# Kernel tuning notes

Measured on AMD Instinct MI355X. Metric: run time of the kernel, lower is better.

## Reference

```python
import jax, jax.numpy as jnp
import numpy as np

B, S, IN, OUT, H, M = 16, 512, 512, 512, 8, 4
HF = OUT // H  # head_feats = 64


def setup_inputs() -> dict:
    key = jax.random.key(0)
    ks = jax.random.split(key, 12)
    std = 0.02
    queries = jax.random.normal(ks[0], (B, S, IN), jnp.float32)
    keys = jax.random.normal(ks[1], (B, S, IN), jnp.float32)
    timespans = jax.random.uniform(ks[2], (B, S), jnp.float32)
    # causal mask tiled over heads*batch, matching [H*B, S, S] score shape
    attention_masks = jnp.broadcast_to(jnp.tril(jnp.ones((S, S), jnp.float32)), (H * B, S, S))
    event_marks = jax.random.uniform(ks[3], (H * B, 1, S, M), jnp.float32)
    Wq = std * jax.random.normal(ks[4], (IN, OUT), jnp.float32)
    Wk = std * jax.random.normal(ks[5], (IN, OUT), jnp.float32)
    Wv = std * jax.random.normal(ks[6], (IN, OUT), jnp.float32)
    Wt = std * jax.random.normal(ks[7], (IN, OUT), jnp.float32)
    Wi = std * jax.random.normal(ks[8], (HF + 1, M * HF), jnp.float32)  # fc_i weight
    bi = jnp.zeros((M * HF,), jnp.float32)                               # fc_i bias
    weight_i = std * jax.random.normal(ks[9], (M, HF), jnp.float32)
    scale_i = jnp.zeros((M,), jnp.float32)
    return {"queries": queries, "keys": keys, "timespans": timespans,
            "attention_masks": attention_masks, "event_marks": event_marks,
            "Wq": Wq, "Wk": Wk, "Wv": Wv, "Wt": Wt, "Wi": Wi, "bi": bi,
            "weight_i": weight_i, "scale_i": scale_i}


def reference(queries, keys, timespans, attention_masks, event_marks,
              Wq, Wk, Wv, Wt, Wi, bi, weight_i, scale_i):
    # torch's cat(chunk(X, H, dim=2), dim=0) == [B,S,H,HF] -> [H,B,S,HF] -> flat h*B+b
    def split_heads(X):
        return X.reshape(B, S, H, HF).transpose(2, 0, 1, 3)  # [H,B,S,HF]

    Q = split_heads(queries @ Wq)
    K = split_heads(keys @ Wk)
    V = split_heads(keys @ Wv)
    T = split_heads(keys @ Wt)

    scores = jnp.einsum('hbqf,hbkf->hbqk', Q, K) / jnp.sqrt(jnp.float32(OUT))
    mask = attention_masks.reshape(H, B, S, S)
    scores = jnp.where(mask == 0.0, jnp.float32(-2 ** 32 + 1), scores)
    attn = jax.nn.softmax(scores, axis=-1)  # [H,B,Sq,Sk]

    E = jnp.einsum('hbqk,hbkf->hbqf', attn, T)  # events fed to intensity net

    # --- Hawkes intensities ---
    ts = jnp.broadcast_to(timespans[None, :, :, None], (H, B, S, 1))
    mu = jax.nn.sigmoid(jnp.concatenate([E, ts], axis=-1) @ Wi + bi)  # [H,B,S,M*HF]
    mu = mu.reshape(H, B, S, M, HF)  # chunk over marks along feature dim
    scale = jnp.exp(scale_i)  # [M]
    lam = jnp.einsum('hbsmf,mf->hbsm', mu, weight_i) / scale
    lam = scale * jnp.log1p(jnp.exp(lam))  # scaled softplus, [H,B,S,M]

    # mark_inty[h,b,q,k] = sum_m lam[h,b,q,m] * event_marks[h,b,k,m]
    em = event_marks.reshape(H, B, S, M)
    mark_inty = jnp.einsum('hbqm,hbkm->hbqk', lam, em)

    out = jnp.einsum('hbqk,hbkf->hbqf', attn * mark_inty, V)
    out = out.transpose(1, 2, 0, 3).reshape(B, S, OUT) + queries[..., :OUT]
    all_mark_inty = lam.reshape(H * B, S, M)
    return out, all_mark_inty
```

## Files before the change

kernel.cpp:

```cpp
#include <hip/hip_runtime.h>
#include <math.h>

typedef __attribute__((ext_vector_type(8))) short short8;
typedef __attribute__((ext_vector_type(4))) float f32x4;

static __device__ __forceinline__ unsigned short f2bf(float f) {
  unsigned int u = __float_as_uint(f);
  u += 0x7FFFu + ((u >> 16) & 1u);
  return (unsigned short)(u >> 16);
}

static __device__ __forceinline__ void cp16(void* lds, const void* g) {
  __builtin_amdgcn_global_load_lds((const __attribute__((address_space(1))) void*)g,
                                   (__attribute__((address_space(3))) void*)lds,
                                   16, 0, 0);
}

__global__ __launch_bounds__(256) void convert_k(
    const float* __restrict__ qin, const float* __restrict__ kin,
    const float* __restrict__ Wq, const float* __restrict__ Wk,
    const float* __restrict__ Wv, const float* __restrict__ Wt,
    const float* __restrict__ Wi,
    unsigned short* __restrict__ qbf, unsigned short* __restrict__ kbf,
    unsigned short* __restrict__ Wb, unsigned short* __restrict__ WiF)
{
  const int blk = blockIdx.x, tid = threadIdx.x;
  if (blk < 8192) {
    const float* src = (blk < 4096) ? qin : kin;
    unsigned short* dst = (blk < 4096) ? qbf : kbf;
    int i = ((blk & 4095) * 256 + tid) * 4;
    float4 v = *(const float4*)(src + i);
    ushort4 o;
    o.x = f2bf(v.x); o.y = f2bf(v.y); o.z = f2bf(v.z); o.w = f2bf(v.w);
    *(ushort4*)(dst + i) = o;
  } else if (blk < 12288) {
    int e = (blk - 8192) * 256 + tid;
    int which = e >> 18;
    int r = (e >> 9) & 511, c = e & 511;
    const float* W = (which == 0) ? Wq : (which == 1) ? Wk : (which == 2) ? Wv : Wt;
    Wb[which * 262144 + c * 512 + r] = f2bf(W[r * 512 + c]);
  } else {
    int e = (blk - 12288) * 256 + tid;
    int j = e & 7, ll = (e >> 3) & 63, r = e >> 9;
    int kk = r % 3, nt = r / 3;
    int col = nt * 16 + (ll & 15);
    int k = kk * 32 + (ll >> 4) * 8 + j;
    float val = (k < 64) ? Wi[k * 256 + col] : ((k == 64) ? Wi[16384 + col] : 0.0f);
    WiF[e] = f2bf(val);
  }
}

__global__ __launch_bounds__(256) void proj_mfma(
    const unsigned short* __restrict__ qin_bf, const unsigned short* __restrict__ kin_bf,
    const unsigned short* __restrict__ Wb,
    unsigned short* __restrict__ Qg, unsigned short* __restrict__ Kg,
    unsigned short* __restrict__ Vt, unsigned short* __restrict__ Tt)
{
  const int which = blockIdx.z;
  const unsigned short* A = (which == 0) ? qin_bf : kin_bf;
  const unsigned short* W = Wb + which * 262144;
  const int row0 = blockIdx.x * 128;
  const int col0 = blockIdx.y * 128;
  const int tid = threadIdx.x;
  const int wv = tid >> 6, l = tid & 63;
  const int quad = l >> 4, lc = l & 15;
  const int wm = wv >> 1, wn = wv & 1;

  __shared__ unsigned short Asm[128 * 32];
  __shared__ unsigned short Bsm[128 * 32];

  f32x4 acc[4][4] = {};
  const int c0 = tid, c1 = tid + 256;

  for (int k0 = 0; k0 < 512; k0 += 32) {
    __syncthreads();
    cp16(&Asm[c0 * 8], A + (size_t)(row0 + (c0 >> 2)) * 512 + k0 + (c0 & 3) * 8);
    cp16(&Asm[c1 * 8], A + (size_t)(row0 + (c1 >> 2)) * 512 + k0 + (c1 & 3) * 8);
    cp16(&Bsm[c0 * 8], W + (size_t)(col0 + (c0 >> 2)) * 512 + k0 + (c0 & 3) * 8);
    cp16(&Bsm[c1 * 8], W + (size_t)(col0 + (c1 >> 2)) * 512 + k0 + (c1 & 3) * 8);
    __syncthreads();
    short8 a[4], b[4];
#pragma unroll
    for (int mi = 0; mi < 4; ++mi)
      a[mi] = *(const short8*)&Asm[(wm * 64 + mi * 16 + lc) * 32 + quad * 8];
#pragma unroll
    for (int nj = 0; nj < 4; ++nj)
      b[nj] = *(const short8*)&Bsm[(wn * 64 + nj * 16 + lc) * 32 + quad * 8];
#pragma unroll
    for (int mi = 0; mi < 4; ++mi)
#pragma unroll
      for (int nj = 0; nj < 4; ++nj)
        acc[mi][nj] = __builtin_amdgcn_mfma_f32_16x16x32_bf16(a[mi], b[nj], acc[mi][nj], 0, 0, 0);
  }

  const int h = (col0 >> 6) + wn;
  const int bidx = row0 >> 9;
  const int hb = h * 16 + bidx;
  if (which < 2) {
    unsigned short* C = (which == 0) ? Qg : Kg;
#pragma unroll
    for (int mi = 0; mi < 4; ++mi) {
      int sbase = (row0 & 511) + wm * 64 + mi * 16 + quad * 4;
#pragma unroll
      for (int nj = 0; nj < 4; ++nj) {
        size_t base = (size_t)hb * 32768 + (size_t)sbase * 64 + nj * 16 + lc;
#pragma unroll
        for (int reg = 0; reg < 4; ++reg)
          C[base + (size_t)reg * 64] = f2bf(acc[mi][nj][reg]);
      }
    }
  } else {
    unsigned short* C = (which == 2) ? Vt : Tt;
#pragma unroll
    for (int mi = 0; mi < 4; ++mi) {
      int sbase = (row0 & 511) + wm * 64 + mi * 16 + quad * 4;
#pragma unroll
      for (int nj = 0; nj < 4; ++nj) {
        ushort4 o;
        o.x = f2bf(acc[mi][nj][0]); o.y = f2bf(acc[mi][nj][1]);
        o.z = f2bf(acc[mi][nj][2]); o.w = f2bf(acc[mi][nj][3]);
        *(ushort4*)&C[(size_t)hb * 32768 + (size_t)(nj * 16 + lc) * 512 + sbase] = o;
      }
    }
  }
}

__global__ __launch_bounds__(256) void attn_passA(
    const unsigned short* __restrict__ Qg, const unsigned short* __restrict__ Kg,
    const unsigned short* __restrict__ Ttg, const float* __restrict__ tsp,
    unsigned short* __restrict__ E96, float* __restrict__ mst, float* __restrict__ lst)
{
  const int qt = blockIdx.x, hb = blockIdx.y;
  const int q0 = qt << 6;
  const int tid = threadIdx.x, wv = tid >> 6, l = tid & 63;
  const int quad = l >> 4, lc = l & 15;

  __shared__ unsigned short Qs[64 * 64];
  __shared__ unsigned short Ks[64 * 64];
  __shared__ unsigned short Ts[64 * 64];
  __shared__ unsigned short Pl[4][16 * 72];

  const unsigned short* Qbase = Qg + (size_t)hb * 32768 + q0 * 64;
  cp16(&Qs[tid * 8], Qbase + tid * 8);
  cp16(&Qs[(tid + 256) * 8], Qbase + (tid + 256) * 8);

  f32x4 Eacc[4] = {};
  float mreg[4], lreg[4];
#pragma unroll
  for (int r = 0; r < 4; ++r) { mreg[r] = -3.0e38f; lreg[r] = 0.0f; }
  const float scl = 0.044194173824159216f;
  const int gqbase = q0 + wv * 16 + quad * 4;

  for (int kt = 0; kt <= qt; ++kt) {
    const int k0 = kt << 6;
    __syncthreads();
    const unsigned short* Kbase = Kg + (size_t)hb * 32768 + k0 * 64;
    cp16(&Ks[tid * 8], Kbase + tid * 8);
    cp16(&Ks[(tid + 256) * 8], Kbase + (tid + 256) * 8);
    const unsigned short* Tbase = Ttg + (size_t)hb * 32768 + k0;
    cp16(&Ts[tid * 8], Tbase + (size_t)(tid >> 3) * 512 + (tid & 7) * 8);
    cp16(&Ts[(tid + 256) * 8], Tbase + (size_t)((tid + 256) >> 3) * 512 + ((tid + 256) & 7) * 8);
    __syncthreads();

    f32x4 sc[4] = {};
#pragma unroll
    for (int kk = 0; kk < 2; ++kk) {
      short8 a = *(const short8*)&Qs[(wv * 16 + lc) * 64 + kk * 32 + quad * 8];
#pragma unroll
      for (int nj = 0; nj < 4; ++nj) {
        short8 b = *(const short8*)&Ks[(nj * 16 + lc) * 64 + kk * 32 + quad * 8];
        sc[nj] = __builtin_amdgcn_mfma_f32_16x16x32_bf16(a, b, sc[nj], 0, 0, 0);
      }
    }
    const bool diag = (kt == qt);
    float sm[4][4], alpha[4];
#pragma unroll
    for (int nj = 0; nj < 4; ++nj)
#pragma unroll
      for (int reg = 0; reg < 4; ++reg) {
        float v = sc[nj][reg] * scl;
        if (diag && (k0 + nj * 16 + lc) > (gqbase + reg)) v = -3.0e38f;
        sm[nj][reg] = v;
      }
#pragma unroll
    for (int reg = 0; reg < 4; ++reg) {
      float tmax = fmaxf(fmaxf(sm[0][reg], sm[1][reg]), fmaxf(sm[2][reg], sm[3][reg]));
#pragma unroll
      for (int off = 1; off < 16; off <<= 1) tmax = fmaxf(tmax, __shfl_xor(tmax, off));
      float mold = mreg[reg];
      float mn = fmaxf(mold, tmax);
      float al = __expf(mold - mn);
      float ts = 0.0f;
#pragma unroll
      for (int nj = 0; nj < 4; ++nj) {
        float p = __expf(sm[nj][reg] - mn);
        sm[nj][reg] = p;
        ts += p;
      }
#pragma unroll
      for (int off = 1; off < 16; off <<= 1) ts += __shfl_xor(ts, off);
      lreg[reg] = lreg[reg] * al + ts;
      mreg[reg] = mn;
      alpha[reg] = al;
    }
#pragma unroll
    for (int fj = 0; fj < 4; ++fj)
#pragma unroll
      for (int reg = 0; reg < 4; ++reg) Eacc[fj][reg] *= alpha[reg];
#pragma unroll
    for (int nj = 0; nj < 4; ++nj)
#pragma unroll
      for (int reg = 0; reg < 4; ++reg)
        Pl[wv][(quad * 4 + reg) * 72 + nj * 16 + lc] = f2bf(sm[nj][reg]);
#pragma unroll
    for (int kk = 0; kk < 2; ++kk) {
      short8 a = *(const short8*)&Pl[wv][lc * 72 + kk * 32 + quad * 8];
#pragma unroll
      for (int fj = 0; fj < 4; ++fj) {
        short8 b = *(const short8*)&Ts[(fj * 16 + lc) * 64 + kk * 32 + quad * 8];
        Eacc[fj] = __builtin_amdgcn_mfma_f32_16x16x32_bf16(a, b, Eacc[fj], 0, 0, 0);
      }
    }
  }

  unsigned short* Eb = E96 + ((size_t)hb * 512 + gqbase) * 96;
#pragma unroll
  for (int reg = 0; reg < 4; ++reg) {
    float inv = 1.0f / lreg[reg];
    unsigned short* rp = Eb + (size_t)reg * 96;
#pragma unroll
    for (int fj = 0; fj < 4; ++fj)
      rp[fj * 16 + lc] = f2bf(Eacc[fj][reg] * inv);
    float tsv = (lc == 0) ? tsp[(hb & 15) * 512 + gqbase + reg] : 0.0f;
    rp[64 + lc] = f2bf(tsv);
    rp[80 + lc] = 0;
  }
  if (lc == 0) {
#pragma unroll
    for (int reg = 0; reg < 4; ++reg) {
      mst[(size_t)hb * 512 + gqbase + reg] = mreg[reg];
      lst[(size_t)hb * 512 + gqbase + reg] = lreg[reg];
    }
  }
}

__global__ __launch_bounds__(256) void intensity_mfma(
    const unsigned short* __restrict__ E96, const unsigned short* __restrict__ WiF,
    const float* __restrict__ bi, const float* __restrict__ wim,
    const float* __restrict__ sci,
    float* __restrict__ lamws, float* __restrict__ lamout)
{
  const int tid = threadIdx.x, wv = tid >> 6, l = tid & 63;
  const int quad = l >> 4, lc = l & 15;
  __shared__ unsigned short WiS[24576];
#pragma unroll
  for (int i = 0; i < 12; ++i)
    cp16(&WiS[(tid + i * 256) * 8], WiF + (tid + i * 256) * 8);

  float bv[16], wmv[16];
#pragma unroll
  for (int nt = 0; nt < 16; ++nt) {
    bv[nt] = bi[nt * 16 + lc];
    wmv[nt] = wim[nt * 16 + lc];
  }
  const float scv = __expf(sci[lc & 3]);
  __syncthreads();

  for (int s = 0; s < 2; ++s) {
    const int row0 = ((blockIdx.x * 4 + wv) * 2 + s) * 16;
    f32x4 acc[16] = {};
#pragma unroll
    for (int kk = 0; kk < 3; ++kk) {
      short8 a = *(const short8*)(E96 + (size_t)(row0 + lc) * 96 + kk * 32 + quad * 8);
#pragma unroll
      for (int nt = 0; nt < 16; ++nt) {
        short8 b = *(const short8*)&WiS[((nt * 3 + kk) * 64 + l) * 8];
        acc[nt] = __builtin_amdgcn_mfma_f32_16x16x32_bf16(a, b, acc[nt], 0, 0, 0);
      }
    }
    float lam4[4][4] = {};
#pragma unroll
    for (int nt = 0; nt < 16; ++nt) {
#pragma unroll
      for (int reg = 0; reg < 4; ++reg) {
        float z = acc[nt][reg] + bv[nt];
        float mu = 1.0f / (1.0f + __expf(-z));
        lam4[reg][nt >> 2] += mu * wmv[nt];
      }
    }
#pragma unroll
    for (int reg = 0; reg < 4; ++reg)
#pragma unroll
      for (int m = 0; m < 4; ++m)
#pragma unroll
        for (int off = 1; off < 16; off <<= 1)
          lam4[reg][m] += __shfl_xor(lam4[reg][m], off);
    if (lc < 4) {
#pragma unroll
      for (int reg = 0; reg < 4; ++reg) {
        float z = lam4[reg][lc] / scv;
        float sp = (z > 20.0f) ? z : log1pf(__expf(z));
        float lv = scv * sp;
        size_t idx = (size_t)(row0 + quad * 4 + reg) * 4 + lc;
        lamws[idx] = lv;
        lamout[idx] = lv;
      }
    }
  }
}

__global__ __launch_bounds__(256) void attn_passB(
    const unsigned short* __restrict__ Qg, const unsigned short* __restrict__ Kg,
    const unsigned short* __restrict__ Vtg,
    const float* __restrict__ mst, const float* __restrict__ lst,
    const float* __restrict__ lam, const float* __restrict__ em,
    const float* __restrict__ queries, float* __restrict__ out)
{
  const int qt = blockIdx.x, hb = blockIdx.y;
  const int q0 = qt << 6;
  const int tid = threadIdx.x, wv = tid >> 6, l = tid & 63;
  const int quad = l >> 4, lc = l & 15;

  __shared__ unsigned short Qs[64 * 64];
  __shared__ unsigned short Ks[64 * 64];
  __shared__ unsigned short Vs[64 * 64];
  __shared__ unsigned short Pl[4][16 * 72];
  __shared__ float emS[64 * 4];

  const unsigned short* Qbase = Qg + (size_t)hb * 32768 + q0 * 64;
  cp16(&Qs[tid * 8], Qbase + tid * 8);
  cp16(&Qs[(tid + 256) * 8], Qbase + (tid + 256) * 8);

  const int gqbase = q0 + wv * 16 + quad * 4;
  float mr[4], li[4];
  float4 lamv[4];
#pragma unroll
  for (int reg = 0; reg < 4; ++reg) {
    size_t r = (size_t)hb * 512 + gqbase + reg;
    mr[reg] = mst[r];
    li[reg] = 1.0f / lst[r];
    lamv[reg] = *(const float4*)&lam[r * 4];
  }
  f32x4 Oacc[4] = {};
  const float scl = 0.044194173824159216f;

  for (int kt = 0; kt <= qt; ++kt) {
    const int k0 = kt << 6;
    __syncthreads();
    const unsigned short* Kbase = Kg + (size_t)hb * 32768 + k0 * 64;
    cp16(&Ks[tid * 8], Kbase + tid * 8);
    cp16(&Ks[(tid + 256) * 8], Kbase + (tid + 256) * 8);
    const unsigned short* Vbase = Vtg + (size_t)hb * 32768 + k0;
    cp16(&Vs[tid * 8], Vbase + (size_t)(tid >> 3) * 512 + (tid & 7) * 8);
    cp16(&Vs[(tid + 256) * 8], Vbase + (size_t)((tid + 256) >> 3) * 512 + ((tid + 256) & 7) * 8);
    emS[tid] = em[(size_t)hb * 2048 + k0 * 4 + tid];
    __syncthreads();

    f32x4 sc[4] = {};
#pragma unroll
    for (int kk = 0; kk < 2; ++kk) {
      short8 a = *(const short8*)&Qs[(wv * 16 + lc) * 64 + kk * 32 + quad * 8];
#pragma unroll
      for (int nj = 0; nj < 4; ++nj) {
        short8 b = *(const short8*)&Ks[(nj * 16 + lc) * 64 + kk * 32 + quad * 8];
        sc[nj] = __builtin_amdgcn_mfma_f32_16x16x32_bf16(a, b, sc[nj], 0, 0, 0);
      }
    }
    const bool diag = (kt == qt);
#pragma unroll
    for (int nj = 0; nj < 4; ++nj) {
      int col = nj * 16 + lc;
      float4 emv = *(const float4*)&emS[col * 4];
#pragma unroll
      for (int reg = 0; reg < 4; ++reg) {
        float v = sc[nj][reg] * scl;
        float p = (diag && (k0 + col) > (gqbase + reg))
                      ? 0.0f : __expf(v - mr[reg]) * li[reg];
        float mk = lamv[reg].x * emv.x + lamv[reg].y * emv.y +
                   lamv[reg].z * emv.z + lamv[reg].w * emv.w;
        Pl[wv][(quad * 4 + reg) * 72 + col] = f2bf(p * mk);
      }
    }
#pragma unroll
    for (int kk = 0; kk < 2; ++kk) {
      short8 a = *(const short8*)&Pl[wv][lc * 72 + kk * 32 + quad * 8];
#pragma unroll
      for (int fj = 0; fj < 4; ++fj) {
        short8 b = *(const short8*)&Vs[(fj * 16 + lc) * 64 + kk * 32 + quad * 8];
        Oacc[fj] = __builtin_amdgcn_mfma_f32_16x16x32_bf16(a, b, Oacc[fj], 0, 0, 0);
      }
    }
  }

  const int h = hb >> 4, bidx = hb & 15;
#pragma unroll
  for (int reg = 0; reg < 4; ++reg) {
    size_t o = (size_t)bidx * 262144 + (size_t)(gqbase + reg) * 512 + h * 64 + lc;
#pragma unroll
    for (int fj = 0; fj < 4; ++fj)
      out[o + fj * 16] = Oacc[fj][reg] + queries[o + fj * 16];
  }
}

extern "C" void kernel_launch(void* const* d_in, const int* in_sizes, int n_in,
                              void* d_out, int out_size, void* d_ws, size_t ws_size,
                              hipStream_t stream)
{
  (void)in_sizes; (void)n_in; (void)out_size; (void)ws_size;
  const float* queries = (const float*)d_in[0];
  const float* keys    = (const float*)d_in[1];
  const float* tsp     = (const float*)d_in[2];
  const float* em      = (const float*)d_in[4];
  const float* Wq      = (const float*)d_in[5];
  const float* Wk      = (const float*)d_in[6];
  const float* Wv      = (const float*)d_in[7];
  const float* Wt      = (const float*)d_in[8];
  const float* Wi      = (const float*)d_in[9];
  const float* bi      = (const float*)d_in[10];
  const float* wim     = (const float*)d_in[11];
  const float* sci     = (const float*)d_in[12];
  float* out = (float*)d_out;

  char* w = (char*)d_ws;
  unsigned short* Qg     = (unsigned short*)(w + 0);
  unsigned short* Kg     = (unsigned short*)(w + 8388608);
  unsigned short* Vt     = (unsigned short*)(w + 16777216);
  unsigned short* Tt     = (unsigned short*)(w + 25165824);
  unsigned short* E96    = (unsigned short*)(w + 33554432);
  float*          mst    = (float*)(w + 46137344);
  float*          lst    = (float*)(w + 46399488);
  float*          lam    = (float*)(w + 46661632);
  unsigned short* qin_bf = (unsigned short*)(w + 47710208);
  unsigned short* kin_bf = (unsigned short*)(w + 56098816);
  unsigned short* Wb     = (unsigned short*)(w + 64487424);
  unsigned short* WiF    = (unsigned short*)(w + 66584576);

  convert_k<<<12384, 256, 0, stream>>>(queries, keys, Wq, Wk, Wv, Wt, Wi,
                                       qin_bf, kin_bf, Wb, WiF);
  proj_mfma<<<dim3(64, 4, 4), 256, 0, stream>>>(qin_bf, kin_bf, Wb, Qg, Kg, Vt, Tt);
  attn_passA<<<dim3(8, 128), 256, 0, stream>>>(Qg, Kg, Tt, tsp, E96, mst, lst);
  intensity_mfma<<<512, 256, 0, stream>>>(E96, WiF, bi, wim, sci,
                                          lam, out + 4194304);
  attn_passB<<<dim3(8, 128), 256, 0, stream>>>(Qg, Kg, Vt, mst, lst, lam, em,
                                               queries, out);
}
```

Measured before the change: 340.6 us.

## Fuse attention pass A, intensity net, and pass B into one balanced causal kernel

Merges the two attention passes and the intensity MLP into one kernel, so the E96, m/l statistics and lambda intermediates never go through global memory and two launches disappear. Each block handles a pair of query tiles (qt and 7-qt) to even out causal work across blocks. It also drops online-softmax max tracking and exponentiates raw scaled scores, relying on scores staying small enough not to overflow. The weight transpose in the conversion kernel now goes through a shared-memory tiled transpose, replacing the strided scalar writes.

```diff
diff --git a/kernel.cpp b/kernel.cpp
--- a/kernel.cpp
+++ b/kernel.cpp
@@ -24,6 +24,7 @@
     unsigned short* __restrict__ qbf, unsigned short* __restrict__ kbf,
     unsigned short* __restrict__ Wb, unsigned short* __restrict__ WiF)
 {
+  __shared__ unsigned short tr[64 * 68];
   const int blk = blockIdx.x, tid = threadIdx.x;
   if (blk < 8192) {
     const float* src = (blk < 4096) ? qin : kin;
@@ -33,14 +34,31 @@
     ushort4 o;
     o.x = f2bf(v.x); o.y = f2bf(v.y); o.z = f2bf(v.z); o.w = f2bf(v.w);
     *(ushort4*)(dst + i) = o;
-  } else if (blk < 12288) {
-    int e = (blk - 8192) * 256 + tid;
-    int which = e >> 18;
-    int r = (e >> 9) & 511, c = e & 511;
+  } else if (blk < 8448) {
+    int t = blk - 8192;
+    int which = t >> 6, tile = t & 63;
+    int r0 = (tile >> 3) << 6, c0 = (tile & 7) << 6;
     const float* W = (which == 0) ? Wq : (which == 1) ? Wk : (which == 2) ? Wv : Wt;
-    Wb[which * 262144 + c * 512 + r] = f2bf(W[r * 512 + c]);
+    const int rr = tid >> 4, cc = (tid & 15) << 2;
+#pragma unroll
+    for (int u = 0; u < 4; ++u) {
+      int r = rr + u * 16;
+      float4 v = *(const float4*)(W + (size_t)(r0 + r) * 512 + c0 + cc);
+      tr[(cc + 0) * 68 + r] = f2bf(v.x);
+      tr[(cc + 1) * 68 + r] = f2bf(v.y);
+      tr[(cc + 2) * 68 + r] = f2bf(v.z);
+      tr[(cc + 3) * 68 + r] = f2bf(v.w);
+    }
+    __syncthreads();
+    unsigned short* dst = Wb + which * 262144;
+#pragma unroll
+    for (int u = 0; u < 4; ++u) {
+      int c = rr + u * 16;
+      ushort4 o = *(const ushort4*)&tr[c * 68 + cc];
+      *(ushort4*)(dst + (size_t)(c0 + c) * 512 + r0 + cc) = o;
+    }
   } else {
-    int e = (blk - 12288) * 256 + tid;
+    int e = (blk - 8448) * 256 + tid;
     int j = e & 7, ll = (e >> 3) & 63, r = e >> 9;
     int kk = r % 3, nt = r / 3;
     int col = nt * 16 + (ll & 15);
@@ -125,280 +143,203 @@
   }
 }
 
-__global__ __launch_bounds__(256) void attn_passA(
+__global__ __launch_bounds__(256) void attn_fused(
     const unsigned short* __restrict__ Qg, const unsigned short* __restrict__ Kg,
-    const unsigned short* __restrict__ Ttg, const float* __restrict__ tsp,
-    unsigned short* __restrict__ E96, float* __restrict__ mst, float* __restrict__ lst)
+    const unsigned short* __restrict__ Vtg, const unsigned short* __restrict__ Ttg,
+    const unsigned short* __restrict__ WiF,
+    const float* __restrict__ bi, const float* __restrict__ wim,
+    const float* __restrict__ sci, const float* __restrict__ tsp,
+    const float* __restrict__ em, const float* __restrict__ queries,
+    float* __restrict__ out, float* __restrict__ lamout)
 {
-  const int qt = blockIdx.x, hb = blockIdx.y;
-  const int q0 = qt << 6;
+  const int hb = blockIdx.y;
   const int tid = threadIdx.x, wv = tid >> 6, l = tid & 63;
   const int quad = l >> 4, lc = l & 15;
 
-  __shared__ unsigned short Qs[64 * 64];
-  __shared__ unsigned short Ks[64 * 64];
-  __shared__ unsigned short Ts[64 * 64];
-  __shared__ unsigned short Pl[4][16 * 72];
-
-  const unsigned short* Qbase = Qg + (size_t)hb * 32768 + q0 * 64;
-  cp16(&Qs[tid * 8], Qbase + tid * 8);
-  cp16(&Qs[(tid + 256) * 8], Qbase + (tid + 256) * 8);
-
-  f32x4 Eacc[4] = {};
-  float mreg[4], lreg[4];
-#pragma unroll
-  for (int r = 0; r < 4; ++r) { mreg[r] = -3.0e38f; lreg[r] = 0.0f; }
+  __shared__ unsigned short Qs[4096];
+  __shared__ unsigned short Ks[4096];
+  __shared__ unsigned short TVs[4096];
+  __shared__ unsigned short Wl[4][16 * 104];
+  __shared__ float emS[256];
+
   const float scl = 0.044194173824159216f;
-  const int gqbase = q0 + wv * 16 + quad * 4;
-
-  for (int kt = 0; kt <= qt; ++kt) {
-    const int k0 = kt << 6;
+  float scm[4];
+#pragma unroll
+  for (int m = 0; m < 4; ++m) scm[m] = __expf(sci[m]);
+
+  for (int half = 0; half < 2; ++half) {
+    const int qt = half ? (7 - blockIdx.x) : blockIdx.x;
+    const int q0 = qt << 6;
+    const int gqbase = q0 + wv * 16 + quad * 4;
     __syncthreads();
-    const unsigned short* Kbase = Kg + (size_t)hb * 32768 + k0 * 64;
-    cp16(&Ks[tid * 8], Kbase + tid * 8);
-    cp16(&Ks[(tid + 256) * 8], Kbase + (tid + 256) * 8);
-    const unsigned short* Tbase = Ttg + (size_t)hb * 32768 + k0;
-    cp16(&Ts[tid * 8], Tbase + (size_t)(tid >> 3) * 512 + (tid & 7) * 8);
-    cp16(&Ts[(tid + 256) * 8], Tbase + (size_t)((tid + 256) >> 3) * 512 + ((tid + 256) & 7) * 8);
-    __syncthreads();
-
-    f32x4 sc[4] = {};
-#pragma unroll
-    for (int kk = 0; kk < 2; ++kk) {
-      short8 a = *(const short8*)&Qs[(wv * 16 + lc) * 64 + kk * 32 + quad * 8];
+    const unsigned short* Qbase = Qg + (size_t)hb * 32768 + q0 * 64;
+    cp16(&Qs[tid * 8], Qbase + tid * 8);
+    cp16(&Qs[(tid + 256) * 8], Qbase + (tid + 256) * 8);
+
+    f32x4 Eacc[4] = {};
+    float lsum[4] = {0.f, 0.f, 0.f, 0.f};
+
+    for (int kt = 0; kt <= qt; ++kt) {
+      const int k0 = kt << 6;
+      __syncthreads();
+      const unsigned short* Kbase = Kg + (size_t)hb * 32768 + k0 * 64;
+      cp16(&Ks[tid * 8], Kbase + tid * 8);
+      cp16(&Ks[(tid + 256) * 8], Kbase + (tid + 256) * 8);
+      const unsigned short* Tbase = Ttg + (size_t)hb * 32768 + k0;
+      cp16(&TVs[tid * 8], Tbase + (size_t)(tid >> 3) * 512 + (tid & 7) * 8);
+      cp16(&TVs[(tid + 256) * 8], Tbase + (size_t)((tid + 256) >> 3) * 512 + ((tid + 256) & 7) * 8);
+      __syncthreads();
+
+      f32x4 sc[4] = {};
+#pragma unroll
+      for (int kk = 0; kk < 2; ++kk) {
+        short8 a = *(const short8*)&Qs[(wv * 16 + lc) * 64 + kk * 32 + quad * 8];
+#pragma unroll
+        for (int nj = 0; nj < 4; ++nj) {
+          short8 b = *(const short8*)&Ks[(nj * 16 + lc) * 64 + kk * 32 + quad * 8];
+          sc[nj] = __builtin_amdgcn_mfma_f32_16x16x32_bf16(a, b, sc[nj], 0, 0, 0);
+        }
+      }
+      const bool diag = (kt == qt);
 #pragma unroll
       for (int nj = 0; nj < 4; ++nj) {
-        short8 b = *(const short8*)&Ks[(nj * 16 + lc) * 64 + kk * 32 + quad * 8];
-        sc[nj] = __builtin_amdgcn_mfma_f32_16x16x32_bf16(a, b, sc[nj], 0, 0, 0);
-      }
-    }
-    const bool diag = (kt == qt);
-    float sm[4][4], alpha[4];
-#pragma unroll
-    for (int nj = 0; nj < 4; ++nj)
+        int col = nj * 16 + lc;
+#pragma unroll
+        for (int reg = 0; reg < 4; ++reg) {
+          float pv = __expf(sc[nj][reg] * scl);
+          if (diag && (k0 + col) > (gqbase + reg)) pv = 0.0f;
+          lsum[reg] += pv;
+          Wl[wv][(quad * 4 + reg) * 104 + col] = f2bf(pv);
+        }
+      }
+#pragma unroll
+      for (int kk = 0; kk < 2; ++kk) {
+        short8 a = *(const short8*)&Wl[wv][lc * 104 + kk * 32 + quad * 8];
+#pragma unroll
+        for (int fj = 0; fj < 4; ++fj) {
+          short8 b = *(const short8*)&TVs[(fj * 16 + lc) * 64 + kk * 32 + quad * 8];
+          Eacc[fj] = __builtin_amdgcn_mfma_f32_16x16x32_bf16(a, b, Eacc[fj], 0, 0, 0);
+        }
+      }
+    }
+
+    float inv[4];
+#pragma unroll
+    for (int reg = 0; reg < 4; ++reg) {
+      float s = lsum[reg];
+#pragma unroll
+      for (int off = 1; off < 16; off <<= 1) s += __shfl_xor(s, off);
+      inv[reg] = 1.0f / s;
+    }
+
+#pragma unroll
+    for (int reg = 0; reg < 4; ++reg) {
+      unsigned short* rp = &Wl[wv][(quad * 4 + reg) * 104];
+#pragma unroll
+      for (int fj = 0; fj < 4; ++fj)
+        rp[fj * 16 + lc] = f2bf(Eacc[fj][reg] * inv[reg]);
+      float tsv = (lc == 0) ? tsp[(hb & 15) * 512 + gqbase + reg] : 0.0f;
+      rp[64 + lc] = f2bf(tsv);
+      rp[80 + lc] = 0;
+    }
+
+    f32x4 iacc[16] = {};
+#pragma unroll
+    for (int kk = 0; kk < 3; ++kk) {
+      short8 a = *(const short8*)&Wl[wv][lc * 104 + kk * 32 + quad * 8];
+#pragma unroll
+      for (int nt = 0; nt < 16; ++nt) {
+        short8 b = *(const short8*)(WiF + ((nt * 3 + kk) * 64 + l) * 8);
+        iacc[nt] = __builtin_amdgcn_mfma_f32_16x16x32_bf16(a, b, iacc[nt], 0, 0, 0);
+      }
+    }
+    float lam4[4][4] = {};
+#pragma unroll
+    for (int nt = 0; nt < 16; ++nt) {
+      float bvv = bi[nt * 16 + lc];
+      float wmv = wim[nt * 16 + lc];
 #pragma unroll
       for (int reg = 0; reg < 4; ++reg) {
-        float v = sc[nj][reg] * scl;
-        if (diag && (k0 + nj * 16 + lc) > (gqbase + reg)) v = -3.0e38f;
-        sm[nj][reg] = v;
-      }
+        float mu = 1.0f / (1.0f + __expf(-(iacc[nt][reg] + bvv)));
+        lam4[reg][nt >> 2] += mu * wmv;
+      }
+    }
+#pragma unroll
+    for (int reg = 0; reg < 4; ++reg)
+#pragma unroll
+      for (int m = 0; m < 4; ++m) {
+        float s = lam4[reg][m];
+#pragma unroll
+        for (int off = 1; off < 16; off <<= 1) s += __shfl_xor(s, off);
+        float z = s / scm[m];
+        float sp = (z > 20.0f) ? z : log1pf(__expf(z));
+        lam4[reg][m] = scm[m] * sp;
+      }
+    if (lc < 4) {
+#pragma unroll
+      for (int reg = 0; reg < 4; ++reg) {
+        float v = (lc == 0) ? lam4[reg][0] : (lc == 1) ? lam4[reg][1]
+                : (lc == 2) ? lam4[reg][2] : lam4[reg][3];
+        lamout[((size_t)hb * 512 + gqbase + reg) * 4 + lc] = v;
+      }
+    }
+
+    f32x4 Oacc[4] = {};
+    for (int kt = 0; kt <= qt; ++kt) {
+      const int k0 = kt << 6;
+      __syncthreads();
+      const unsigned short* Kbase = Kg + (size_t)hb * 32768 + k0 * 64;
+      cp16(&Ks[tid * 8], Kbase + tid * 8);
+      cp16(&Ks[(tid + 256) * 8], Kbase + (tid + 256) * 8);
+      const unsigned short* Vbase = Vtg + (size_t)hb * 32768 + k0;
+      cp16(&TVs[tid * 8], Vbase + (size_t)(tid >> 3) * 512 + (tid & 7) * 8);
+      cp16(&TVs[(tid + 256) * 8], Vbase + (size_t)((tid + 256) >> 3) * 512 + ((tid + 256) & 7) * 8);
+      emS[tid] = em[(size_t)hb * 2048 + k0 * 4 + tid];
+      __syncthreads();
+
+      f32x4 sc[4] = {};
+#pragma unroll
+      for (int kk = 0; kk < 2; ++kk) {
+        short8 a = *(const short8*)&Qs[(wv * 16 + lc) * 64 + kk * 32 + quad * 8];
+#pragma unroll
+        for (int nj = 0; nj < 4; ++nj) {
+          short8 b = *(const short8*)&Ks[(nj * 16 + lc) * 64 + kk * 32 + quad * 8];
+          sc[nj] = __builtin_amdgcn_mfma_f32_16x16x32_bf16(a, b, sc[nj], 0, 0, 0);
+        }
+      }
+      const bool diag = (kt == qt);
+#pragma unroll
+      for (int nj = 0; nj < 4; ++nj) {
+        int col = nj * 16 + lc;
+        float4 emv = *(const float4*)&emS[col * 4];
+#pragma unroll
+        for (int reg = 0; reg < 4; ++reg) {
+          float pv = (diag && (k0 + col) > (gqbase + reg))
+                         ? 0.0f : __expf(sc[nj][reg] * scl) * inv[reg];
+          float mk = lam4[reg][0] * emv.x + lam4[reg][1] * emv.y +
+                     lam4[reg][2] * emv.z + lam4[reg][3] * emv.w;
+          Wl[wv][(quad * 4 + reg) * 104 + col] = f2bf(pv * mk);
+        }
+      }
+#pragma unroll
+      for (int kk = 0; kk < 2; ++kk) {
+        short8 a = *(const short8*)&Wl[wv][lc * 104 + kk * 32 + quad * 8];
+#pragma unroll
+        for (int fj = 0; fj < 4; ++fj) {
+          short8 b = *(const short8*)&TVs[(fj * 16 + lc) * 64 + kk * 32 + quad * 8];
+          Oacc[fj] = __builtin_amdgcn_mfma_f32_16x16x32_bf16(a, b, Oacc[fj], 0, 0, 0);
+        }
+      }
+    }
+
+    const int h = hb >> 4, bidx = hb & 15;
 #pragma unroll
     for (int reg = 0; reg < 4; ++reg) {
-      float tmax = fmaxf(fmaxf(sm[0][reg], sm[1][reg]), fmaxf(sm[2][reg], sm[3][reg]));
-#pragma unroll
-      for (int off = 1; off < 16; off <<= 1) tmax = fmaxf(tmax, __shfl_xor(tmax, off));
-      float mold = mreg[reg];
-      float mn = fmaxf(mold, tmax);
-      float al = __expf(mold - mn);
-      float ts = 0.0f;
-#pragma unroll
-      for (int nj = 0; nj < 4; ++nj) {
-        float p = __expf(sm[nj][reg] - mn);
-        sm[nj][reg] = p;
-        ts += p;
-      }
-#pragma unroll
-      for (int off = 1; off < 16; off <<= 1) ts += __shfl_xor(ts, off);
-      lreg[reg] = lreg[reg] * al + ts;
-      mreg[reg] = mn;
-      alpha[reg] = al;
-    }
-#pragma unroll
-    for (int fj = 0; fj < 4; ++fj)
-#pragma unroll
-      for (int reg = 0; reg < 4; ++reg) Eacc[fj][reg] *= alpha[reg];
-#pragma unroll
-    for (int nj = 0; nj < 4; ++nj)
-#pragma unroll
-      for (int reg = 0; reg < 4; ++reg)
-        Pl[wv][(quad * 4 + reg) * 72 + nj * 16 + lc] = f2bf(sm[nj][reg]);
-#pragma unroll
-    for (int kk = 0; kk < 2; ++kk) {
-      short8 a = *(const short8*)&Pl[wv][lc * 72 + kk * 32 + quad * 8];
-#pragma unroll
-      for (int fj = 0; fj < 4; ++fj) {
-        short8 b = *(const short8*)&Ts[(fj * 16 + lc) * 64 + kk * 32 + quad * 8];
-        Eacc[fj] = __builtin_amdgcn_mfma_f32_16x16x32_bf16(a, b, Eacc[fj], 0, 0, 0);
-      }
-    }
-  }
-
-  unsigned short* Eb = E96 + ((size_t)hb * 512 + gqbase) * 96;
-#pragma unroll
-  for (int reg = 0; reg < 4; ++reg) {
-    float inv = 1.0f / lreg[reg];
-    unsigned short* rp = Eb + (size_t)reg * 96;
-#pragma unroll
-    for (int fj = 0; fj < 4; ++fj)
-      rp[fj * 16 + lc] = f2bf(Eacc[fj][reg] * inv);
-    float tsv = (lc == 0) ? tsp[(hb & 15) * 512 + gqbase + reg] : 0.0f;
-    rp[64 + lc] = f2bf(tsv);
-    rp[80 + lc] = 0;
-  }
-  if (lc == 0) {
-#pragma unroll
-    for (int reg = 0; reg < 4; ++reg) {
-      mst[(size_t)hb * 512 + gqbase + reg] = mreg[reg];
-      lst[(size_t)hb * 512 + gqbase + reg] = lreg[reg];
-    }
-  }
-}
-
-__global__ __launch_bounds__(256) void intensity_mfma(
-    const unsigned short* __restrict__ E96, const unsigned short* __restrict__ WiF,
-    const float* __restrict__ bi, const float* __restrict__ wim,
-    const float* __restrict__ sci,
-    float* __restrict__ lamws, float* __restrict__ lamout)
-{
-  const int tid = threadIdx.x, wv = tid >> 6, l = tid & 63;
-  const int quad = l >> 4, lc = l & 15;
-  __shared__ unsigned short WiS[24576];
-#pragma unroll
-  for (int i = 0; i < 12; ++i)
-    cp16(&WiS[(tid + i * 256) * 8], WiF + (tid + i * 256) * 8);
-
-  float bv[16], wmv[16];
-#pragma unroll
-  for (int nt = 0; nt < 16; ++nt) {
-    bv[nt] = bi[nt * 16 + lc];
-    wmv[nt] = wim[nt * 16 + lc];
-  }
-  const float scv = __expf(sci[lc & 3]);
-  __syncthreads();
-
-  for (int s = 0; s < 2; ++s) {
-    const int row0 = ((blockIdx.x * 4 + wv) * 2 + s) * 16;
-    f32x4 acc[16] = {};
-#pragma unroll
-    for (int kk = 0; kk < 3; ++kk) {
-      short8 a = *(const short8*)(E96 + (size_t)(row0 + lc) * 96 + kk * 32 + quad * 8);
-#pragma unroll
-      for (int nt = 0; nt < 16; ++nt) {
-        short8 b = *(const short8*)&WiS[((nt * 3 + kk) * 64 + l) * 8];
-        acc[nt] = __builtin_amdgcn_mfma_f32_16x16x32_bf16(a, b, acc[nt], 0, 0, 0);
-      }
-    }
-    float lam4[4][4] = {};
-#pragma unroll
-    for (int nt = 0; nt < 16; ++nt) {
-#pragma unroll
-      for (int reg = 0; reg < 4; ++reg) {
-        float z = acc[nt][reg] + bv[nt];
-        float mu = 1.0f / (1.0f + __expf(-z));
-        lam4[reg][nt >> 2] += mu * wmv[nt];
-      }
-    }
-#pragma unroll
-    for (int reg = 0; reg < 4; ++reg)
-#pragma unroll
-      for (int m = 0; m < 4; ++m)
-#pragma unroll
-        for (int off = 1; off < 16; off <<= 1)
-          lam4[reg][m] += __shfl_xor(lam4[reg][m], off);
-    if (lc < 4) {
-#pragma unroll
-      for (int reg = 0; reg < 4; ++reg) {
-        float z = lam4[reg][lc] / scv;
-        float sp = (z > 20.0f) ? z : log1pf(__expf(z));
-        float lv = scv * sp;
-        size_t idx = (size_t)(row0 + quad * 4 + reg) * 4 + lc;
-        lamws[idx] = lv;
-        lamout[idx] = lv;
-      }
-    }
-  }
-}
-
-__global__ __launch_bounds__(256) void attn_passB(
-    const unsigned short* __restrict__ Qg, const unsigned short* __restrict__ Kg,
-    const unsigned short* __restrict__ Vtg,
-    const float* __restrict__ mst, const float* __restrict__ lst,
-    const float* __restrict__ lam, const float* __restrict__ em,
-    const float* __restrict__ queries, float* __restrict__ out)
-{
-  const int qt = blockIdx.x, hb = blockIdx.y;
-  const int q0 = qt << 6;
-  const int tid = threadIdx.x, wv = tid >> 6, l = tid & 63;
-  const int quad = l >> 4, lc = l & 15;
-
-  __shared__ unsigned short Qs[64 * 64];
-  __shared__ unsigned short Ks[64 * 64];
-  __shared__ unsigned short Vs[64 * 64];
-  __shared__ unsigned short Pl[4][16 * 72];
-  __shared__ float emS[64 * 4];
-
-  const unsigned short* Qbase = Qg + (size_t)hb * 32768 + q0 * 64;
-  cp16(&Qs[tid * 8], Qbase + tid * 8);
-  cp16(&Qs[(tid + 256) * 8], Qbase + (tid + 256) * 8);
-
-  const int gqbase = q0 + wv * 16 + quad * 4;
-  float mr[4], li[4];
-  float4 lamv[4];
-#pragma unroll
-  for (int reg = 0; reg < 4; ++reg) {
-    size_t r = (size_t)hb * 512 + gqbase + reg;
-    mr[reg] = mst[r];
-    li[reg] = 1.0f / lst[r];
-    lamv[reg] = *(const float4*)&lam[r * 4];
-  }
-  f32x4 Oacc[4] = {};
-  const float scl = 0.044194173824159216f;
-
-  for (int kt = 0; kt <= qt; ++kt) {
-    const int k0 = kt << 6;
-    __syncthreads();
-    const unsigned short* Kbase = Kg + (size_t)hb * 32768 + k0 * 64;
-    cp16(&Ks[tid * 8], Kbase + tid * 8);
-    cp16(&Ks[(tid + 256) * 8], Kbase + (tid + 256) * 8);
-    const unsigned short* Vbase = Vtg + (size_t)hb * 32768 + k0;
-    cp16(&Vs[tid * 8], Vbase + (size_t)(tid >> 3) * 512 + (tid & 7) * 8);
-    cp16(&Vs[(tid + 256) * 8], Vbase + (size_t)((tid + 256) >> 3) * 512 + ((tid + 256) & 7) * 8);
-    emS[tid] = em[(size_t)hb * 2048 + k0 * 4 + tid];
-    __syncthreads();
-
-    f32x4 sc[4] = {};
-#pragma unroll
-    for (int kk = 0; kk < 2; ++kk) {
-      short8 a = *(const short8*)&Qs[(wv * 16 + lc) * 64 + kk * 32 + quad * 8];
-#pragma unroll
-      for (int nj = 0; nj < 4; ++nj) {
-        short8 b = *(const short8*)&Ks[(nj * 16 + lc) * 64 + kk * 32 + quad * 8];
-        sc[nj] = __builtin_amdgcn_mfma_f32_16x16x32_bf16(a, b, sc[nj], 0, 0, 0);
-      }
-    }
-    const bool diag = (kt == qt);
-#pragma unroll
-    for (int nj = 0; nj < 4; ++nj) {
-      int col = nj * 16 + lc;
-      float4 emv = *(const float4*)&emS[col * 4];
-#pragma unroll
-      for (int reg = 0; reg < 4; ++reg) {
-        float v = sc[nj][reg] * scl;
-        float p = (diag && (k0 + col) > (gqbase + reg))
-                      ? 0.0f : __expf(v - mr[reg]) * li[reg];
-        float mk = lamv[reg].x * emv.x + lamv[reg].y * emv.y +
-                   lamv[reg].z * emv.z + lamv[reg].w * emv.w;
-        Pl[wv][(quad * 4 + reg) * 72 + col] = f2bf(p * mk);
-      }
-    }
-#pragma unroll
-    for (int kk = 0; kk < 2; ++kk) {
-      short8 a = *(const short8*)&Pl[wv][lc * 72 + kk * 32 + quad * 8];
-#pragma unroll
-      for (int fj = 0; fj < 4; ++fj) {
-        short8 b = *(const short8*)&Vs[(fj * 16 + lc) * 64 + kk * 32 + quad * 8];
-        Oacc[fj] = __builtin_amdgcn_mfma_f32_16x16x32_bf16(a, b, Oacc[fj], 0, 0, 0);
-      }
-    }
-  }
-
-  const int h = hb >> 4, bidx = hb & 15;
-#pragma unroll
-  for (int reg = 0; reg < 4; ++reg) {
-    size_t o = (size_t)bidx * 262144 + (size_t)(gqbase + reg) * 512 + h * 64 + lc;
-#pragma unroll
-    for (int fj = 0; fj < 4; ++fj)
-      out[o + fj * 16] = Oacc[fj][reg] + queries[o + fj * 16];
+      size_t o = (size_t)bidx * 262144 + (size_t)(gqbase + reg) * 512 + h * 64 + lc;
+#pragma unroll
+      for (int fj = 0; fj < 4; ++fj)
+        out[o + fj * 16] = Oacc[fj][reg] + queries[o + fj * 16];
+    }
   }
 }
 
@@ -426,21 +367,15 @@
   unsigned short* Kg     = (unsigned short*)(w + 8388608);
   unsigned short* Vt     = (unsigned short*)(w + 16777216);
   unsigned short* Tt     = (unsigned short*)(w + 25165824);
-  unsigned short* E96    = (unsigned short*)(w + 33554432);
-  float*          mst    = (float*)(w + 46137344);
-  float*          lst    = (float*)(w + 46399488);
-  float*          lam    = (float*)(w + 46661632);
-  unsigned short* qin_bf = (unsigned short*)(w + 47710208);
-  unsigned short* kin_bf = (unsigned short*)(w + 56098816);
-  unsigned short* Wb     = (unsigned short*)(w + 64487424);
-  unsigned short* WiF    = (unsigned short*)(w + 66584576);
-
-  convert_k<<<12384, 256, 0, stream>>>(queries, keys, Wq, Wk, Wv, Wt, Wi,
-                                       qin_bf, kin_bf, Wb, WiF);
+  unsigned short* qin_bf = (unsigned short*)(w + 33554432);
+  unsigned short* kin_bf = (unsigned short*)(w + 41943040);
+  unsigned short* Wb     = (unsigned short*)(w + 50331648);
+  unsigned short* WiF    = (unsigned short*)(w + 52428800);
+
+  convert_k<<<8544, 256, 0, stream>>>(queries, keys, Wq, Wk, Wv, Wt, Wi,
+                                      qin_bf, kin_bf, Wb, WiF);
   proj_mfma<<<dim3(64, 4, 4), 256, 0, stream>>>(qin_bf, kin_bf, Wb, Qg, Kg, Vt, Tt);
-  attn_passA<<<dim3(8, 128), 256, 0, stream>>>(Qg, Kg, Tt, tsp, E96, mst, lst);
-  intensity_mfma<<<512, 256, 0, stream>>>(E96, WiF, bi, wim, sci,
-                                          lam, out + 4194304);
-  attn_passB<<<dim3(8, 128), 256, 0, stream>>>(Qg, Kg, Vt, mst, lst, lam, em,
-                                               queries, out);
-}
+  attn_fused<<<dim3(4, 128), 256, 0, stream>>>(Qg, Kg, Vt, Tt, WiF, bi, wim, sci,
+                                               tsp, em, queries, out,
+                                               out + 4194304);
+}
```

After: 355.3 us. 4.3% more time.
